# Kernel optimization log

Hardware: AMD Instinct MI355X
Metric: run time of the kernel (lower is better)

## Reference

```python
import jax, jax.numpy as jnp
import numpy as np

NUM_USERS = 100000
NUM_ITEMS = 50000
N_NODES = NUM_USERS + NUM_ITEMS
LATENT_DIM = 64
N_LAYERS = 3
N_EDGES = 4800000


def setup_inputs() -> dict:
    key = jax.random.key(0)
    ks = jax.random.split(key, 7)
    user_emb = jax.random.normal(ks[0], (NUM_USERS, LATENT_DIM), dtype=jnp.float32) * 0.1
    item_emb = jax.random.normal(ks[1], (NUM_ITEMS, LATENT_DIM), dtype=jnp.float32) * 0.1
    edge_src = jax.random.randint(ks[2], (N_EDGES,), 0, N_NODES, dtype=jnp.int32)
    edge_dst = jax.random.randint(ks[3], (N_EDGES,), 0, N_NODES, dtype=jnp.int32)
    # normalized adjacency values (positive, ~1/deg scale)
    edge_vals = jax.random.uniform(ks[4], (N_EDGES,), dtype=jnp.float32) * 0.05
    users = jax.random.randint(ks[5], (1024,), 0, NUM_USERS, dtype=jnp.int32)
    items = jax.random.randint(ks[6], (20000,), 0, NUM_ITEMS, dtype=jnp.int32)
    return {"user_emb": user_emb, "item_emb": item_emb,
            "edge_src": edge_src, "edge_dst": edge_dst, "edge_vals": edge_vals,
            "users": users, "items": items}


def _spmm(edge_src, edge_dst, edge_vals, x):
    # y[dst] += vals * x[src]  == sparse.mm(Graph, x)
    msgs = edge_vals[:, None] * x[edge_src]           # [E, D]
    return jax.ops.segment_sum(msgs, edge_dst, num_segments=N_NODES)


def reference(user_emb, item_emb, edge_src, edge_dst, edge_vals, users, items):
    all_em = jnp.concatenate([user_emb, item_emb], axis=0)  # [N, D]
    acc = all_em  # running sum over layers (mean at the end)
    h = all_em
    for _ in range(N_LAYERS):
        h = _spmm(edge_src, edge_dst, edge_vals, h)
        acc = acc + h
    result = acc / jnp.float32(N_LAYERS + 1)  # mean over stacked layers
    all_users = result[:NUM_USERS]
    all_items = result[NUM_USERS:]
    u = all_users[users]        # [Bu, D]
    it = all_items[items]       # [Bi, D]
    ratings = jax.nn.sigmoid(jnp.matmul(u, it.T))  # [Bu, Bi]
    return ratings
```

## Files before the change

### kernel.cpp

```cpp
#include <hip/hip_runtime.h>
#include <hip/hip_bf16.h>

#define NUM_USERS 100000
#define NUM_ITEMS 50000
#define N_NODES   150000
#define DIM       64
#define N_LAYERS  3
#define N_QU      1024
#define N_QI      20000
#define N_QTOT    (N_QU + N_QI)
#define SLOTS     80

#define BIN_SHIFT 9
#define BIN_W     512
#define NBINS     ((N_NODES + BIN_W - 1) >> BIN_SHIFT)
#define BIN_CAP   17472
#define S1_BATCH  2048

typedef __attribute__((ext_vector_type(8))) short bf16x8;
typedef __attribute__((ext_vector_type(4))) float f32x4;
typedef __attribute__((ext_vector_type(8))) unsigned short u16x8;

__device__ __forceinline__ short f2bf(float x) {
    unsigned u = __float_as_uint(x);
    u += 0x7FFF + ((u >> 16) & 1);
    return (short)(u >> 16);
}
__device__ __forceinline__ float bf2f(unsigned short u) {
    return __uint_as_float((unsigned)u << 16);
}

__global__ void init_h0(const float* __restrict__ ue, const float* __restrict__ ie,
                        unsigned short* __restrict__ h0) {
    const size_t n8   = (size_t)N_NODES * DIM / 8;
    const size_t uend = (size_t)NUM_USERS * DIM / 8;
    size_t stride = (size_t)gridDim.x * blockDim.x;
    for (size_t i = (size_t)blockIdx.x * blockDim.x + threadIdx.x; i < n8; i += stride) {
        const float4* s = (i < uend) ? ((const float4*)ue) + i * 2
                                     : ((const float4*)ie) + (i - uend) * 2;
        float4 a = s[0], b = s[1];
        ushort4 lo, hi;
        lo.x = (unsigned short)f2bf(a.x); lo.y = (unsigned short)f2bf(a.y);
        lo.z = (unsigned short)f2bf(a.z); lo.w = (unsigned short)f2bf(a.w);
        hi.x = (unsigned short)f2bf(b.x); hi.y = (unsigned short)f2bf(b.y);
        hi.z = (unsigned short)f2bf(b.z); hi.w = (unsigned short)f2bf(b.w);
        ((ushort4*)h0)[i * 2]     = lo;
        ((ushort4*)h0)[i * 2 + 1] = hi;
    }
}

__global__ void build_qlist(const int* __restrict__ users, const int* __restrict__ items,
                            int* __restrict__ qlist) {
    int i = blockIdx.x * blockDim.x + threadIdx.x;
    if (i < N_QU) qlist[i] = users[i];
    else if (i < N_QTOT) qlist[i] = NUM_USERS + items[i - N_QU];
}

__global__ __launch_bounds__(256) void s1_coarse(
        const int* __restrict__ src, const int* __restrict__ dst,
        const float* __restrict__ vals, int* __restrict__ gcnt,
        int2* __restrict__ binned, int n) {
    __shared__ int dcache[S1_BATCH];
    __shared__ int hist[NBINS];
    __shared__ int base[NBINS];
    const int t  = threadIdx.x;
    const int b0 = blockIdx.x * S1_BATCH;

    for (int i = t; i < NBINS; i += 256) hist[i] = 0;
    __syncthreads();

    #pragma unroll
    for (int k = 0; k < S1_BATCH / 256; ++k) {
        int e = b0 + k * 256 + t;
        int d = (e < n) ? dst[e] : -1;
        dcache[k * 256 + t] = d;
        if (d >= 0) atomicAdd(&hist[d >> BIN_SHIFT], 1);
    }
    __syncthreads();

    for (int i = t; i < NBINS; i += 256) {
        int c = hist[i];
        base[i] = (c > 0) ? atomicAdd(&gcnt[i], c) : 0;
        hist[i] = 0;
    }
    __syncthreads();

    #pragma unroll
    for (int k = 0; k < S1_BATCH / 256; ++k) {
        int e = b0 + k * 256 + t;
        if (e < n) {
            int d   = dcache[k * 256 + t];
            int bin = d >> BIN_SHIFT;
            int local = atomicAdd(&hist[bin], 1);
            int slot  = base[bin] + local;
            if (slot < BIN_CAP) {
                int w0 = ((d & (BIN_W - 1)) << 18) | src[e];
                binned[(size_t)bin * BIN_CAP + slot] =
                    make_int2(w0, __float_as_int(vals[e]));
            }
        }
    }
}

__global__ __launch_bounds__(1024) void s2_fine(
        const int* __restrict__ gcnt, const int2* __restrict__ binned,
        int* __restrict__ cnt, int2* __restrict__ buckets) {
    __shared__ int cursor[BIN_W];
    const int bin = blockIdx.x;
    const int t   = threadIdx.x;
    if (t < BIN_W) cursor[t] = 0;
    __syncthreads();

    int m = gcnt[bin]; if (m > BIN_CAP) m = BIN_CAP;
    const int2* bp = &binned[(size_t)bin * BIN_CAP];
    for (int i = t; i < m; i += 1024) {
        int2 p  = bp[i];
        int  dl = ((unsigned)p.x) >> 18;
        int  local = atomicAdd(&cursor[dl], 1);
        if (local < SLOTS) {
            int node = (bin << BIN_SHIFT) + dl;
            buckets[(size_t)node * SLOTS + local] =
                make_int2(p.x & 0x3FFFF, p.y);
        }
    }
    __syncthreads();

    if (t < BIN_W) {
        int node = (bin << BIN_SHIFT) + t;
        if (node < N_NODES) {
            int c = cursor[t]; if (c > SLOTS) c = SLOTS;
            cnt[node] = c;
        }
    }
}

__global__ __launch_bounds__(256) void spmm_bucket_bf16(
        const int* __restrict__ cnt, const int2* __restrict__ buckets,
        const unsigned short* __restrict__ x, unsigned short* __restrict__ y,
        const int* __restrict__ list, int count) {
    int lane8   = threadIdx.x & 7;
    int group   = (int)((blockIdx.x * blockDim.x + threadIdx.x) >> 3);
    int ngroups = (int)((gridDim.x * blockDim.x) >> 3);
    const u16x8* x8 = (const u16x8*)x;

    int i = group;
    if (i >= count) return;
    int node_n = list ? list[i] : i;
    int m_n = cnt[node_n];

    for (; i < count; i += ngroups) {
        int node = node_n;
        int m = m_n; if (m > SLOTS) m = SLOTS;
        int j = i + ngroups;
        if (j < count) { node_n = list ? list[j] : j; m_n = cnt[node_n]; }

        const int2* row  = &buckets[(size_t)node * SLOTS];
        const int4* row2 = (const int4*)row;
        float r[8];
        #pragma unroll
        for (int k = 0; k < 8; ++k) r[k] = 0.0f;

        int e = 0;
        for (; e + 4 <= m; e += 4) {
            int4 pa = row2[(e >> 1)];
            int4 pb = row2[(e >> 1) + 1];
            u16x8 x0 = x8[(size_t)pa.x * 8 + lane8];
            u16x8 x1 = x8[(size_t)pa.z * 8 + lane8];
            u16x8 x2 = x8[(size_t)pb.x * 8 + lane8];
            u16x8 x3 = x8[(size_t)pb.z * 8 + lane8];
            float v0 = __int_as_float(pa.y), v1 = __int_as_float(pa.w);
            float v2 = __int_as_float(pb.y), v3 = __int_as_float(pb.w);
            #pragma unroll
            for (int k = 0; k < 8; ++k) r[k] += v0 * bf2f(x0[k]);
            #pragma unroll
            for (int k = 0; k < 8; ++k) r[k] += v1 * bf2f(x1[k]);
            #pragma unroll
            for (int k = 0; k < 8; ++k) r[k] += v2 * bf2f(x2[k]);
            #pragma unroll
            for (int k = 0; k < 8; ++k) r[k] += v3 * bf2f(x3[k]);
        }
        if (e + 2 <= m) {
            int4 pa = row2[(e >> 1)];
            u16x8 x0 = x8[(size_t)pa.x * 8 + lane8];
            u16x8 x1 = x8[(size_t)pa.z * 8 + lane8];
            float v0 = __int_as_float(pa.y), v1 = __int_as_float(pa.w);
            #pragma unroll
            for (int k = 0; k < 8; ++k) r[k] += v0 * bf2f(x0[k]);
            #pragma unroll
            for (int k = 0; k < 8; ++k) r[k] += v1 * bf2f(x1[k]);
            e += 2;
        }
        if (e < m) {
            int2 p = row[e];
            float v = __int_as_float(p.y);
            u16x8 x0 = x8[(size_t)p.x * 8 + lane8];
            #pragma unroll
            for (int k = 0; k < 8; ++k) r[k] += v * bf2f(x0[k]);
        }

        u16x8 o;
        #pragma unroll
        for (int k = 0; k < 8; ++k) o[k] = (unsigned short)f2bf(r[k]);
        ((u16x8*)y)[(size_t)node * 8 + lane8] = o;
    }
}

__global__ __launch_bounds__(256) void prep_packed(
        const float* __restrict__ ue, const float* __restrict__ ie,
        const unsigned short* __restrict__ h1, const unsigned short* __restrict__ h2,
        const unsigned short* __restrict__ h3, const int* __restrict__ users,
        const int* __restrict__ items, unsigned short* __restrict__ packed) {
    int idx = blockIdx.x * blockDim.x + threadIdx.x;
    if (idx >= N_QTOT * 8) return;
    int q = idx >> 3, lane = idx & 7;

    const float* e0;
    size_t hoff;
    if (q < N_QU) {
        int u = users[q];
        e0   = &ue[(size_t)u * DIM];
        hoff = (size_t)u * DIM;
    } else {
        int it = items[q - N_QU];
        e0   = &ie[(size_t)it * DIM];
        hoff = (size_t)(NUM_USERS + it) * DIM;
    }
    int d0 = lane * 8;
    const float4* s0 = (const float4*)&e0[d0];
    float4 a0 = s0[0], a1 = s0[1];
    u16x8 b1 = *(const u16x8*)&h1[hoff + d0];
    u16x8 b2 = *(const u16x8*)&h2[hoff + d0];
    u16x8 b3 = *(const u16x8*)&h3[hoff + d0];

    float v[8];
    v[0] = a0.x; v[1] = a0.y; v[2] = a0.z; v[3] = a0.w;
    v[4] = a1.x; v[5] = a1.y; v[6] = a1.z; v[7] = a1.w;
    u16x8 o;
    #pragma unroll
    for (int k = 0; k < 8; ++k) {
        float t = (v[k] + bf2f(b1[k]) + bf2f(b2[k]) + bf2f(b3[k])) * 0.25f;
        o[k] = (unsigned short)f2bf(t);
    }
    *(u16x8*)&packed[(size_t)q * DIM + d0] = o;
}

__global__ __launch_bounds__(256) void rating_mfma(
        const unsigned short* __restrict__ packed, float* __restrict__ out) {
    __shared__ short Ut[64 * 72];
    __shared__ short Tt[256 * 72];
    const int bj = blockIdx.x;
    const int bi = blockIdx.y;
    const int tid = threadIdx.x;

    {
        int r = tid >> 2, c16 = (tid & 3) * 16;
        const bf16x8* s = (const bf16x8*)&packed[(size_t)(bi * 64 + r) * DIM + c16];
        *(bf16x8*)&Ut[r * 72 + c16]     = s[0];
        *(bf16x8*)&Ut[r * 72 + c16 + 8] = s[1];
    }

    #pragma unroll
    for (int p = 0; p < 4; ++p) {
        int r = (tid >> 2) + p * 64, c16 = (tid & 3) * 16;
        int jg = bj * 256 + r;
        bf16x8 lo = (bf16x8)(short)0, hi = (bf16x8)(short)0;
        if (jg < N_QI) {
            const bf16x8* s = (const bf16x8*)&packed[(size_t)(N_QU + jg) * DIM + c16];
            lo = s[0]; hi = s[1];
        }
        *(bf16x8*)&Tt[r * 72 + c16]     = lo;
        *(bf16x8*)&Tt[r * 72 + c16 + 8] = hi;
    }
    __syncthreads();

    const int wv = tid >> 6, lane = tid & 63;
    const int lr = lane & 15, kq = lane >> 4;

    f32x4 c[4][4];
    #pragma unroll
    for (int mr = 0; mr < 4; ++mr)
        #pragma unroll
        for (int nr = 0; nr < 4; ++nr)
            c[mr][nr] = (f32x4)(0.0f);

    #pragma unroll
    for (int kb = 0; kb < 2; ++kb) {
        bf16x8 a[4], b[4];
        #pragma unroll
        for (int mr = 0; mr < 4; ++mr)
            a[mr] = *(const bf16x8*)&Ut[(mr * 16 + lr) * 72 + (kb * 4 + kq) * 8];
        #pragma unroll
        for (int nr = 0; nr < 4; ++nr)
            b[nr] = *(const bf16x8*)&Tt[(wv * 64 + nr * 16 + lr) * 72 + (kb * 4 + kq) * 8];
        #pragma unroll
        for (int mr = 0; mr < 4; ++mr)
            #pragma unroll
            for (int nr = 0; nr < 4; ++nr)
                c[mr][nr] = __builtin_amdgcn_mfma_f32_16x16x32_bf16(a[mr], b[nr], c[mr][nr], 0, 0, 0);
    }

    #pragma unroll
    for (int mr = 0; mr < 4; ++mr) {
        int rowg = bi * 64 + mr * 16 + kq * 4;
        #pragma unroll
        for (int nr = 0; nr < 4; ++nr) {
            int colg = bj * 256 + wv * 64 + nr * 16 + lr;
            if (colg < N_QI) {
                #pragma unroll
                for (int q = 0; q < 4; ++q) {
                    float z = c[mr][nr][q];
                    out[(size_t)(rowg + q) * N_QI + colg] = 1.0f / (1.0f + __expf(-z));
                }
            }
        }
    }
}

extern "C" void kernel_launch(void* const* d_in, const int* in_sizes, int n_in,
                              void* d_out, int out_size, void* d_ws, size_t ws_size,
                              hipStream_t stream) {
    const float* user_emb  = (const float*)d_in[0];
    const float* item_emb  = (const float*)d_in[1];
    const int*   edge_src  = (const int*)d_in[2];
    const int*   edge_dst  = (const int*)d_in[3];
    const float* edge_vals = (const float*)d_in[4];
    const int*   users     = (const int*)d_in[5];
    const int*   items     = (const int*)d_in[6];
    float*       out       = (float*)d_out;
    int n_edges = in_sizes[2];

    const size_t nodeElems = (size_t)N_NODES * DIM;

    unsigned short* h0 = (unsigned short*)d_ws;
    unsigned short* h1 = h0 + nodeElems;
    unsigned short* h2 = h1 + nodeElems;
    unsigned short* h3 = h2 + nodeElems;
    int*  cnt     = (int*)(h3 + nodeElems);
    int2* buckets = (int2*)(cnt + N_NODES);
    int*  qlist   = (int*)(buckets + (size_t)N_NODES * SLOTS);
    unsigned short* packed = (unsigned short*)(qlist + N_QTOT);
    int*  gcnt    = (int*)(packed + (size_t)N_QTOT * DIM);
    int2* binned  = (int2*)h1;

    (void)hipMemsetAsync(gcnt, 0, NBINS * sizeof(int), stream);
    init_h0<<<2048, 256, 0, stream>>>(user_emb, item_emb, h0);
    build_qlist<<<(N_QTOT + 255) / 256, 256, 0, stream>>>(users, items, qlist);

    int nbatches = (n_edges + S1_BATCH - 1) / S1_BATCH;
    s1_coarse<<<nbatches, 256, 0, stream>>>(edge_src, edge_dst, edge_vals,
                                            gcnt, binned, n_edges);
    s2_fine<<<NBINS, 1024, 0, stream>>>(gcnt, binned, cnt, buckets);

    spmm_bucket_bf16<<<2048, 256, 0, stream>>>(cnt, buckets, h0, h1, nullptr, N_NODES);
    spmm_bucket_bf16<<<2048, 256, 0, stream>>>(cnt, buckets, h1, h2, nullptr, N_NODES);
    spmm_bucket_bf16<<<2048, 256, 0, stream>>>(cnt, buckets, h2, h3, qlist, N_QTOT);

    prep_packed<<<(N_QTOT * 8 + 255) / 256, 256, 0, stream>>>(
        user_emb, item_emb, h1, h2, h3, users, items, packed);

    dim3 grid((N_QI + 255) / 256, N_QU / 64);
    rating_mfma<<<grid, 256, 0, stream>>>(packed, out);
}
```

Baseline: 422.0 us.

## Stage coarse-binned edges in shared memory and write them out coalesced per bin

The coarse binning kernel doubles its batch size and loads dst/src/vals as 4-wide vectors. It now computes a block-local prefix sum over the bin histogram and scatters edges into a shared-memory staging buffer sorted by bin. Each wave then copies contiguous per-bin runs to global memory, replacing the scattered 8-byte global writes with mostly coalesced ones. The cost is 32KB of LDS per block, which lowers occupancy, and extra barriers for the scan.

```diff
diff --git a/kernel.cpp b/kernel.cpp
--- a/kernel.cpp
+++ b/kernel.cpp
@@ -15,7 +15,7 @@
 #define BIN_W     512
 #define NBINS     ((N_NODES + BIN_W - 1) >> BIN_SHIFT)
 #define BIN_CAP   17472
-#define S1_BATCH  2048
+#define S1_BATCH  4096
 
 typedef __attribute__((ext_vector_type(8))) short bf16x8;
 typedef __attribute__((ext_vector_type(4))) float f32x4;
@@ -60,43 +60,104 @@
         const int* __restrict__ src, const int* __restrict__ dst,
         const float* __restrict__ vals, int* __restrict__ gcnt,
         int2* __restrict__ binned, int n) {
-    __shared__ int dcache[S1_BATCH];
-    __shared__ int hist[NBINS];
-    __shared__ int base[NBINS];
+    __shared__ int2 staging[S1_BATCH];
+    __shared__ int  hist[NBINS];
+    __shared__ int  base[NBINS];
+    __shared__ int  pfx[NBINS];
+    __shared__ int  part[256];
     const int t  = threadIdx.x;
     const int b0 = blockIdx.x * S1_BATCH;
+    const int n4 = n >> 2;
+    const int i4base = b0 >> 2;
+    const int4*   d4 = (const int4*)dst;
+    const int4*   s4 = (const int4*)src;
+    const float4* v4 = (const float4*)vals;
 
     for (int i = t; i < NBINS; i += 256) hist[i] = 0;
     __syncthreads();
 
     #pragma unroll
-    for (int k = 0; k < S1_BATCH / 256; ++k) {
-        int e = b0 + k * 256 + t;
-        int d = (e < n) ? dst[e] : -1;
-        dcache[k * 256 + t] = d;
-        if (d >= 0) atomicAdd(&hist[d >> BIN_SHIFT], 1);
+    for (int k = 0; k < 4; ++k) {
+        int i4 = i4base + k * 256 + t;
+        if (i4 < n4) {
+            int4 d = d4[i4];
+            atomicAdd(&hist[d.x >> BIN_SHIFT], 1);
+            atomicAdd(&hist[d.y >> BIN_SHIFT], 1);
+            atomicAdd(&hist[d.z >> BIN_SHIFT], 1);
+            atomicAdd(&hist[d.w >> BIN_SHIFT], 1);
+        }
+    }
+    for (int e = (n & ~3) + t; e < n; e += 256)
+        if (e >= b0 && e < b0 + S1_BATCH)
+            atomicAdd(&hist[dst[e] >> BIN_SHIFT], 1);
+    __syncthreads();
+
+    {
+        int i0 = 2 * t, i1 = 2 * t + 1;
+        int h0v = (i0 < NBINS) ? hist[i0] : 0;
+        int h1v = (i1 < NBINS) ? hist[i1] : 0;
+        int s = h0v + h1v;
+        part[t] = s;
+        __syncthreads();
+        int x = s;
+        for (int off = 1; off < 256; off <<= 1) {
+            int y = (t >= off) ? part[t - off] : 0;
+            __syncthreads();
+            x += y;
+            part[t] = x;
+            __syncthreads();
+        }
+        int exc = x - s;
+        if (i0 < NBINS) pfx[i0] = exc;
+        if (i1 < NBINS) pfx[i1] = exc + h0v;
     }
     __syncthreads();
 
     for (int i = t; i < NBINS; i += 256) {
         int c = hist[i];
         base[i] = (c > 0) ? atomicAdd(&gcnt[i], c) : 0;
-        hist[i] = 0;
-    }
-    __syncthreads();
-
-    #pragma unroll
-    for (int k = 0; k < S1_BATCH / 256; ++k) {
-        int e = b0 + k * 256 + t;
-        if (e < n) {
-            int d   = dcache[k * 256 + t];
+    }
+    __syncthreads();
+    for (int i = t; i < NBINS; i += 256) hist[i] = 0;
+    __syncthreads();
+
+    #pragma unroll
+    for (int k = 0; k < 4; ++k) {
+        int i4 = i4base + k * 256 + t;
+        if (i4 < n4) {
+            int4   d = d4[i4];
+            int4   s = s4[i4];
+            float4 v = v4[i4];
+            int bin, loc;
+            bin = d.x >> BIN_SHIFT; loc = atomicAdd(&hist[bin], 1);
+            staging[pfx[bin] + loc] = make_int2(((d.x & (BIN_W-1)) << 18) | s.x, __float_as_int(v.x));
+            bin = d.y >> BIN_SHIFT; loc = atomicAdd(&hist[bin], 1);
+            staging[pfx[bin] + loc] = make_int2(((d.y & (BIN_W-1)) << 18) | s.y, __float_as_int(v.y));
+            bin = d.z >> BIN_SHIFT; loc = atomicAdd(&hist[bin], 1);
+            staging[pfx[bin] + loc] = make_int2(((d.z & (BIN_W-1)) << 18) | s.z, __float_as_int(v.z));
+            bin = d.w >> BIN_SHIFT; loc = atomicAdd(&hist[bin], 1);
+            staging[pfx[bin] + loc] = make_int2(((d.w & (BIN_W-1)) << 18) | s.w, __float_as_int(v.w));
+        }
+    }
+    for (int e = (n & ~3) + t; e < n; e += 256)
+        if (e >= b0 && e < b0 + S1_BATCH) {
+            int d = dst[e];
             int bin = d >> BIN_SHIFT;
-            int local = atomicAdd(&hist[bin], 1);
-            int slot  = base[bin] + local;
-            if (slot < BIN_CAP) {
-                int w0 = ((d & (BIN_W - 1)) << 18) | src[e];
-                binned[(size_t)bin * BIN_CAP + slot] =
-                    make_int2(w0, __float_as_int(vals[e]));
+            int loc = atomicAdd(&hist[bin], 1);
+            staging[pfx[bin] + loc] = make_int2(((d & (BIN_W-1)) << 18) | src[e], __float_as_int(vals[e]));
+        }
+    __syncthreads();
+
+    {
+        int wid = t >> 6, lane = t & 63;
+        for (int bin = wid; bin < NBINS; bin += 4) {
+            int c = hist[bin];
+            int g = base[bin];
+            int p = pfx[bin];
+            for (int l = lane; l < c; l += 64) {
+                int slot = g + l;
+                if (slot < BIN_CAP)
+                    binned[(size_t)bin * BIN_CAP + slot] = staging[p + l];
             }
         }
     }
```

New measurement: 360.7 us. -14.5%, faster.
